# Kernel tuning notes

Hardware: AMD Instinct MI355X
Metric: run time of the kernel (lower is better)

The kernel has to match this reference:

```python
import jax, jax.numpy as jnp
import numpy as np

EMB_LEN = 16384
EMB_DIM = 128
BETA = 0.25
WEIGHT_DECAY = 0.01


def resize_linear(x, axis, out_size):
    # PyTorch (tri)linear interpolation, align_corners=False, separable per axis.
    in_size = x.shape[axis]
    if in_size == out_size:
        return x
    src = (jnp.arange(out_size, dtype=jnp.float32) + 0.5) * (in_size / out_size) - 0.5
    src = jnp.clip(src, 0.0, in_size - 1.0)
    i0 = jnp.floor(src).astype(jnp.int32)
    i1 = jnp.minimum(i0 + 1, in_size - 1)
    w1 = src - i0.astype(jnp.float32)
    x0 = jnp.take(x, i0, axis=axis)
    x1 = jnp.take(x, i1, axis=axis)
    bshape = [1] * x.ndim
    bshape[axis] = out_size
    w1 = w1.reshape(bshape)
    return x0 * (1.0 - w1) + x1 * w1


def setup_inputs() -> dict:
    key = jax.random.key(0)
    k1, k2 = jax.random.split(key)
    b, c, h, w = 16384, 16, 2, 4  # h*w must equal 8 (see shape analysis)
    z = jax.random.normal(k1, (b, c, h, w), dtype=jnp.float32)
    emb_weight = jax.random.uniform(
        k2, (EMB_LEN, EMB_DIM), dtype=jnp.float32,
        minval=-1.0 / EMB_LEN, maxval=1.0 / EMB_LEN)
    return {"z": z, "emb_weight": emb_weight}


def reference(z, emb_weight):
    b, c, h, w = z.shape
    # feature_unfolding: F.interpolate(x, 2, mode='trilinear') -> size=(2,2,2)
    x = z[:, :, None, :, :]                       # [b,c,1,h,w]
    x = resize_linear(x, 2, 2)                    # depth 1 -> 2 (duplicate)
    x = resize_linear(x, 3, 2)                    # h -> 2
    x = resize_linear(x, 4, 2)                    # w -> 2
    # pixelshuffle3D_downscale(scale=2) on [b,c,2,2,2] -> [b,8c,1,1,1];
    # flatten order matches contiguous reshape.
    zf = x.reshape(b, c * 8)                      # [b, emb_dim]
    # squared L2 distance via expansion
    d = (jnp.sum(zf ** 2, axis=1, keepdims=True)
         + jnp.sum(emb_weight ** 2, axis=1)
         - 2.0 * zf @ emb_weight.T)               # [b, emb_len]
    idx = jnp.argmin(d, axis=1)                   # [b]
    z_q = emb_weight[idx].reshape(b, c, h, w)
    sg = jax.lax.stop_gradient
    commit = BETA * jnp.mean((sg(z_q) - z) ** 2) + jnp.mean((z_q - sg(z)) ** 2)
    zd = sg(z)
    vx = z_q - jnp.mean(z_q)
    vy = zd - jnp.mean(zd)
    pearson = 0.5 + 0.5 * jnp.sum(vx * vy) / (
        jnp.sqrt(jnp.sum(vx ** 2)) * jnp.sqrt(jnp.sum(vy ** 2)))
    # torch.linalg.norm(W, ord=1) on 2D matrix = max column abs-sum
    reg = WEIGHT_DECAY * jnp.max(jnp.sum(jnp.abs(emb_weight), axis=0))
    loss = commit + pearson + reg
    z_q_out = z + sg(z_q - z)                     # straight-through
    # rearrange 'b h w c -> b c h w' on a [b,c,h,w] tensor == permute(0,3,1,2)
    z_q_out = jnp.transpose(z_q_out, (0, 3, 1, 2))
    return z_q_out, loss, idx
```

## Files before the change

### kernel.cpp

```cpp
#include <hip/hip_runtime.h>
#include <cstdint>
#include <cstddef>

#define B_ROWS 16384
#define EMB_LEN 16384
#define K_DIM 128
#define JSPLIT 8
#define JLEN (EMB_LEN / JSPLIT)
#define RB 32
#define JT 256
#define KC 16

typedef const __attribute__((address_space(1))) void* gas_vp;
typedef __attribute__((address_space(3))) void* las_vp;

__device__ __forceinline__ void dma16(const float* g, float* l) {
    __builtin_amdgcn_global_load_lds((gas_vp)g, (las_vp)l, 16, 0, 0);
}

__global__ void zf_kernel(const float* __restrict__ z,
                          float* __restrict__ zf, float* __restrict__ Cb) {
    int b = blockIdx.x;
    int i = threadIdx.x;
    int c = i >> 3, h = (i >> 1) & 1, wp = i & 1;
    const float* zr = z + (size_t)b * 128 + c * 8 + h * 4 + wp * 2;
    float v = 0.5f * zr[0] + 0.5f * zr[1];
    zf[(size_t)b * 128 + i] = v;
    float s = v * v;
    for (int o = 32; o; o >>= 1) s += __shfl_down(s, o, 64);
    __shared__ float sm[2];
    if ((threadIdx.x & 63) == 0) sm[threadIdx.x >> 6] = s;
    __syncthreads();
    if (threadIdx.x == 0) Cb[b] = sm[0] + sm[1];
}

__global__ void transpose_kernel(const float* __restrict__ emb,
                                 float* __restrict__ embT) {
    __shared__ float t[128][65];
    int j0 = blockIdx.x * 64;
    int jl = threadIdx.x >> 2;
    int kq = threadIdx.x & 3;
    const float* er = emb + (size_t)(j0 + jl) * 128;
#pragma unroll
    for (int q = 0; q < 8; ++q) {
        int k4 = (kq * 8 + q) * 4;
        float4 v = *(const float4*)(er + k4);
        t[k4 + 0][jl] = v.x;
        t[k4 + 1][jl] = v.y;
        t[k4 + 2][jl] = v.z;
        t[k4 + 3][jl] = v.w;
    }
    __syncthreads();
    int kk = threadIdx.x >> 4;
    int jl4 = (threadIdx.x & 15) * 4;
#pragma unroll
    for (int q = 0; q < 8; ++q) {
        int k = kk + q * 16;
        float4 v = make_float4(t[k][jl4], t[k][jl4 + 1], t[k][jl4 + 2], t[k][jl4 + 3]);
        *(float4*)(embT + (size_t)k * EMB_LEN + j0 + jl4) = v;
    }
}

#define FMA_ROW(cr, av) \
    cr.x = fmaf(av, bv.x, cr.x); \
    cr.y = fmaf(av, bv.y, cr.y); \
    cr.z = fmaf(av, bv.z, cr.z); \
    cr.w = fmaf(av, bv.w, cr.w);

#define UPD(rr, cr) { \
    float dv0 = cb##rr - 2.0f * cr.x; \
    float dv1 = cb##rr - 2.0f * cr.y; \
    float dv2 = cb##rr - 2.0f * cr.z; \
    float dv3 = cb##rr - 2.0f * cr.w; \
    if (dv0 < bd##rr) { bd##rr = dv0; bj##rr = jb; } \
    if (dv1 < bd##rr) { bd##rr = dv1; bj##rr = jb + 1; } \
    if (dv2 < bd##rr) { bd##rr = dv2; bj##rr = jb + 2; } \
    if (dv3 < bd##rr) { bd##rr = dv3; bj##rr = jb + 3; } \
}

#define RED(rr) { \
    float bd = bd##rr; int bj = bj##rr; \
    for (int o = 32; o; o >>= 1) { \
        float d2 = __shfl_down(bd, o, 64); \
        int j2 = __shfl_down(bj, o, 64); \
        if (d2 < bd || (d2 == bd && j2 < bj)) { bd = d2; bj = j2; } \
    } \
    if (l == 0) { \
        cand_d[sp * B_ROWS + rbase + w8 + rr] = bd; \
        cand_j[sp * B_ROWS + rbase + w8 + rr] = bj; \
    } \
}

__global__ void argmin_kernel(const float* __restrict__ zf,
                              const float* __restrict__ Cb,
                              const float* __restrict__ embT,
                              float* __restrict__ cand_d,
                              int* __restrict__ cand_j) {
    __shared__ float zfs[K_DIM][RB + 4];
    __shared__ float es[2][KC][JT];

    int sp = blockIdx.x & 7;
    int rb = blockIdx.x >> 3;
    int rbase = rb * RB;
    int jbase = sp * JLEN;
    int tid = threadIdx.x;
    int w = tid >> 6;
    int l = tid & 63;
    int w8 = w << 3;
    int l4 = l << 2;

    {
        int r0 = tid >> 3;
        int kq0 = tid & 7;
        const float* zr = zf + (size_t)(rbase + r0) * K_DIM;
        for (int kq = kq0; kq < 32; kq += 8) {
            float4 v = *(const float4*)(zr + kq * 4);
            zfs[kq * 4 + 0][r0] = v.x;
            zfs[kq * 4 + 1][r0] = v.y;
            zfs[kq * 4 + 2][r0] = v.z;
            zfs[kq * 4 + 3][r0] = v.w;
        }
    }

    const float* cbp = Cb + rbase + w8;
    float cb0 = cbp[0], cb1 = cbp[1], cb2 = cbp[2], cb3 = cbp[3];
    float cb4 = cbp[4], cb5 = cbp[5], cb6 = cbp[6], cb7 = cbp[7];

    float bd0 = 3.4e38f, bd1 = 3.4e38f, bd2 = 3.4e38f, bd3 = 3.4e38f;
    float bd4 = 3.4e38f, bd5 = 3.4e38f, bd6 = 3.4e38f, bd7 = 3.4e38f;
    int bj0 = 0, bj1 = 0, bj2 = 0, bj3 = 0, bj4 = 0, bj5 = 0, bj6 = 0, bj7 = 0;

    {
        const float* gb = embT + jbase + l4;
        float* lb = &es[0][w][0];
        dma16(gb + (size_t)(0 + w) * EMB_LEN, lb + 0 * JT);
        dma16(gb + (size_t)(4 + w) * EMB_LEN, lb + 4 * JT);
        dma16(gb + (size_t)(8 + w) * EMB_LEN, lb + 8 * JT);
        dma16(gb + (size_t)(12 + w) * EMB_LEN, lb + 12 * JT);
    }

    int buf = 0;
    for (int jt = 0; jt < JLEN; jt += JT) {
        float4 c0 = make_float4(0.f, 0.f, 0.f, 0.f);
        float4 c1 = make_float4(0.f, 0.f, 0.f, 0.f);
        float4 c2 = make_float4(0.f, 0.f, 0.f, 0.f);
        float4 c3 = make_float4(0.f, 0.f, 0.f, 0.f);
        float4 c4 = make_float4(0.f, 0.f, 0.f, 0.f);
        float4 c5 = make_float4(0.f, 0.f, 0.f, 0.f);
        float4 c6 = make_float4(0.f, 0.f, 0.f, 0.f);
        float4 c7 = make_float4(0.f, 0.f, 0.f, 0.f);

        for (int kc = 0; kc < K_DIM; kc += KC) {
            __syncthreads();

            {
                int kc2 = kc + KC, jt2 = jt;
                if (kc2 == K_DIM) { kc2 = 0; jt2 += JT; }
                if (jt2 < JLEN) {
                    const float* gb = embT + (size_t)kc2 * EMB_LEN + jbase + jt2 + l4;
                    float* lb = &es[buf ^ 1][w][0];
                    dma16(gb + (size_t)(0 + w) * EMB_LEN, lb + 0 * JT);
                    dma16(gb + (size_t)(4 + w) * EMB_LEN, lb + 4 * JT);
                    dma16(gb + (size_t)(8 + w) * EMB_LEN, lb + 8 * JT);
                    dma16(gb + (size_t)(12 + w) * EMB_LEN, lb + 12 * JT);
                }
            }

            const float (*eb)[JT] = es[buf];
#pragma unroll
            for (int k = 0; k < KC; ++k) {
                const float4 bv = *(const float4*)(&eb[k][l4]);
                const float4 a0 = *(const float4*)(&zfs[kc + k][w8]);
                const float4 a1 = *(const float4*)(&zfs[kc + k][w8 + 4]);
                FMA_ROW(c0, a0.x)
                FMA_ROW(c1, a0.y)
                FMA_ROW(c2, a0.z)
                FMA_ROW(c3, a0.w)
                FMA_ROW(c4, a1.x)
                FMA_ROW(c5, a1.y)
                FMA_ROW(c6, a1.z)
                FMA_ROW(c7, a1.w)
            }
            buf ^= 1;
        }

        int jb = jbase + jt + l4;
        UPD(0, c0)
        UPD(1, c1)
        UPD(2, c2)
        UPD(3, c3)
        UPD(4, c4)
        UPD(5, c5)
        UPD(6, c6)
        UPD(7, c7)
    }

    RED(0)
    RED(1)
    RED(2)
    RED(3)
    RED(4)
    RED(5)
    RED(6)
    RED(7)
}

__global__ void merge_kernel(const float* __restrict__ cand_d,
                             const int* __restrict__ cand_j,
                             int* __restrict__ idxw,
                             float* __restrict__ out_idx) {
    int b = blockIdx.x * 256 + threadIdx.x;
    float bd = cand_d[b];
    int bj = cand_j[b];
#pragma unroll
    for (int s = 1; s < JSPLIT; ++s) {
        float d = cand_d[s * B_ROWS + b];
        int j = cand_j[s * B_ROWS + b];
        if (d < bd) { bd = d; bj = j; }
    }
    idxw[b] = bj;
    out_idx[b] = (float)bj;
}

__global__ void output_kernel(const float* __restrict__ z,
                              const float* __restrict__ emb,
                              const int* __restrict__ idxw,
                              float* __restrict__ out,
                              double* __restrict__ accs) {
    int stride = gridDim.x * blockDim.x;
    double s[6] = {0, 0, 0, 0, 0, 0};
    for (int n = blockIdx.x * blockDim.x + threadIdx.x; n < B_ROWS * 128; n += stride) {
        int b = n >> 7, i = n & 127;
        int c = i >> 3, h = (i >> 2) & 1, w = i & 3;
        float zv = z[n];
        float qv = emb[(size_t)idxw[b] * 128 + i];
        float diff = qv - zv;
        out[(size_t)((b * 4 + w) * 16 + c) * 2 + h] = zv + diff;
        s[0] += (double)qv;
        s[1] += (double)zv;
        s[2] += (double)qv * qv;
        s[3] += (double)zv * zv;
        s[4] += (double)qv * zv;
        s[5] += (double)diff * diff;
    }
    int lane = threadIdx.x & 63, wv = threadIdx.x >> 6;
#pragma unroll
    for (int q = 0; q < 6; ++q)
        for (int o = 32; o; o >>= 1) s[q] += __shfl_down(s[q], o, 64);
    __shared__ double sm[6][4];
    if (lane == 0)
#pragma unroll
        for (int q = 0; q < 6; ++q) sm[q][wv] = s[q];
    __syncthreads();
    if (threadIdx.x == 0) {
#pragma unroll
        for (int q = 0; q < 6; ++q)
            atomicAdd(&accs[q], sm[q][0] + sm[q][1] + sm[q][2] + sm[q][3]);
    }
}

__global__ void colsum_kernel(const float* __restrict__ emb, float* __restrict__ colsum) {
    int j = blockIdx.x;
    double s = 0;
    for (int i = threadIdx.x; i < EMB_LEN; i += blockDim.x)
        s += (double)fabsf(emb[(size_t)i * 128 + j]);
    int lane = threadIdx.x & 63, wv = threadIdx.x >> 6;
    for (int o = 32; o; o >>= 1) s += __shfl_down(s, o, 64);
    __shared__ double sm[4];
    if (lane == 0) sm[wv] = s;
    __syncthreads();
    if (threadIdx.x == 0) colsum[j] = (float)(sm[0] + sm[1] + sm[2] + sm[3]);
}

__global__ void loss_kernel(const double* __restrict__ accs,
                            const float* __restrict__ colsum,
                            float* __restrict__ out_loss) {
    __shared__ float sm[128];
    int tid = threadIdx.x;
    sm[tid] = colsum[tid];
    __syncthreads();
    for (int s = 64; s; s >>= 1) {
        if (tid < s) sm[tid] = fmaxf(sm[tid], sm[tid + s]);
        __syncthreads();
    }
    if (tid == 0) {
        double n = (double)B_ROWS * 128.0;
        double m = accs[5] / n;
        double commit = 0.25 * m + m;
        double Sx = accs[0], Sy = accs[1], Sxx = accs[2], Syy = accs[3], Sxy = accs[4];
        double cov = Sxy - Sx * Sy / n;
        double vx = Sxx - Sx * Sx / n;
        double vy = Syy - Sy * Sy / n;
        double pearson = 0.5 + 0.5 * cov / (sqrt(vx) * sqrt(vy));
        double reg = 0.01 * (double)sm[0];
        out_loss[0] = (float)(commit + pearson + reg);
    }
}

extern "C" void kernel_launch(void* const* d_in, const int* in_sizes, int n_in,
                              void* d_out, int out_size, void* d_ws, size_t ws_size,
                              hipStream_t stream) {
    const float* z = (const float*)d_in[0];
    const float* emb = (const float*)d_in[1];
    float* out = (float*)d_out;

    float* zf = (float*)d_ws;
    float* embT = zf + 2097152;
    float* Cb = embT + 2097152;
    float* cand_d = Cb + 16384;
    int* cand_j = (int*)(cand_d + JSPLIT * B_ROWS);
    int* idxw = cand_j + JSPLIT * B_ROWS;
    double* accs = (double*)(idxw + 16384);
    float* colsum = (float*)(accs + 8);

    hipMemsetAsync(accs, 0, 8 * sizeof(double), stream);

    zf_kernel<<<B_ROWS, 128, 0, stream>>>(z, zf, Cb);
    transpose_kernel<<<EMB_LEN / 64, 256, 0, stream>>>(emb, embT);
    argmin_kernel<<<512 * JSPLIT, 256, 0, stream>>>(zf, Cb, embT, cand_d, cand_j);
    merge_kernel<<<B_ROWS / 256, 256, 0, stream>>>(cand_d, cand_j, idxw, out + 2097153);
    output_kernel<<<1024, 256, 0, stream>>>(z, emb, idxw, out, accs);
    colsum_kernel<<<128, 256, 0, stream>>>(emb, colsum);
    loss_kernel<<<1, 128, 0, stream>>>(accs, colsum, out + 2097152);
}
```

Baseline: 990.7 us.

## Enlarge argmin register tile to 16 rows per wave with KC halved

Doubles the rows handled per block (RB 32→64), so each wave keeps a 16×4 accumulator tile instead of 8×4. Each loaded embedding value is reused across twice as many rows, halving global embedding traffic per row. KC drops to 8 to keep the LDS footprint in check, and the per-row norms move to shared memory to save registers. The cost is higher register pressure (64 accumulators plus 16 best-distance/index pairs), which lowers occupancy, and twice as many barriers per tile.

```diff
diff --git a/kernel.cpp b/kernel.cpp
--- a/kernel.cpp
+++ b/kernel.cpp
@@ -7,9 +7,9 @@
 #define K_DIM 128
 #define JSPLIT 8
 #define JLEN (EMB_LEN / JSPLIT)
-#define RB 32
+#define RB 64
 #define JT 256
-#define KC 16
+#define KC 8
 
 typedef const __attribute__((address_space(1))) void* gas_vp;
 typedef __attribute__((address_space(3))) void* las_vp;
@@ -68,10 +68,11 @@
     cr.w = fmaf(av, bv.w, cr.w);
 
 #define UPD(rr, cr) { \
-    float dv0 = cb##rr - 2.0f * cr.x; \
-    float dv1 = cb##rr - 2.0f * cr.y; \
-    float dv2 = cb##rr - 2.0f * cr.z; \
-    float dv3 = cb##rr - 2.0f * cr.w; \
+    float cbr = cbs[w16 + rr]; \
+    float dv0 = cbr - 2.0f * cr.x; \
+    float dv1 = cbr - 2.0f * cr.y; \
+    float dv2 = cbr - 2.0f * cr.z; \
+    float dv3 = cbr - 2.0f * cr.w; \
     if (dv0 < bd##rr) { bd##rr = dv0; bj##rr = jb; } \
     if (dv1 < bd##rr) { bd##rr = dv1; bj##rr = jb + 1; } \
     if (dv2 < bd##rr) { bd##rr = dv2; bj##rr = jb + 2; } \
@@ -86,8 +87,8 @@
         if (d2 < bd || (d2 == bd && j2 < bj)) { bd = d2; bj = j2; } \
     } \
     if (l == 0) { \
-        cand_d[sp * B_ROWS + rbase + w8 + rr] = bd; \
-        cand_j[sp * B_ROWS + rbase + w8 + rr] = bj; \
+        cand_d[sp * B_ROWS + rbase + w16 + rr] = bd; \
+        cand_j[sp * B_ROWS + rbase + w16 + rr] = bj; \
     } \
 }
 
@@ -98,6 +99,7 @@
                               int* __restrict__ cand_j) {
     __shared__ float zfs[K_DIM][RB + 4];
     __shared__ float es[2][KC][JT];
+    __shared__ float cbs[RB];
 
     int sp = blockIdx.x & 7;
     int rb = blockIdx.x >> 3;
@@ -106,37 +108,34 @@
     int tid = threadIdx.x;
     int w = tid >> 6;
     int l = tid & 63;
-    int w8 = w << 3;
+    int w16 = w << 4;
     int l4 = l << 2;
 
     {
-        int r0 = tid >> 3;
-        int kq0 = tid & 7;
+        int r0 = tid >> 2;
+        int kq0 = tid & 3;
         const float* zr = zf + (size_t)(rbase + r0) * K_DIM;
-        for (int kq = kq0; kq < 32; kq += 8) {
+        for (int kq = kq0; kq < 32; kq += 4) {
             float4 v = *(const float4*)(zr + kq * 4);
             zfs[kq * 4 + 0][r0] = v.x;
             zfs[kq * 4 + 1][r0] = v.y;
             zfs[kq * 4 + 2][r0] = v.z;
             zfs[kq * 4 + 3][r0] = v.w;
         }
-    }
-
-    const float* cbp = Cb + rbase + w8;
-    float cb0 = cbp[0], cb1 = cbp[1], cb2 = cbp[2], cb3 = cbp[3];
-    float cb4 = cbp[4], cb5 = cbp[5], cb6 = cbp[6], cb7 = cbp[7];
+        if (tid < RB) cbs[tid] = Cb[rbase + tid];
+    }
 
     float bd0 = 3.4e38f, bd1 = 3.4e38f, bd2 = 3.4e38f, bd3 = 3.4e38f;
     float bd4 = 3.4e38f, bd5 = 3.4e38f, bd6 = 3.4e38f, bd7 = 3.4e38f;
+    float bd8 = 3.4e38f, bd9 = 3.4e38f, bd10 = 3.4e38f, bd11 = 3.4e38f;
+    float bd12 = 3.4e38f, bd13 = 3.4e38f, bd14 = 3.4e38f, bd15 = 3.4e38f;
     int bj0 = 0, bj1 = 0, bj2 = 0, bj3 = 0, bj4 = 0, bj5 = 0, bj6 = 0, bj7 = 0;
+    int bj8 = 0, bj9 = 0, bj10 = 0, bj11 = 0, bj12 = 0, bj13 = 0, bj14 = 0, bj15 = 0;
 
     {
         const float* gb = embT + jbase + l4;
-        float* lb = &es[0][w][0];
-        dma16(gb + (size_t)(0 + w) * EMB_LEN, lb + 0 * JT);
-        dma16(gb + (size_t)(4 + w) * EMB_LEN, lb + 4 * JT);
-        dma16(gb + (size_t)(8 + w) * EMB_LEN, lb + 8 * JT);
-        dma16(gb + (size_t)(12 + w) * EMB_LEN, lb + 12 * JT);
+        dma16(gb + (size_t)(2 * w) * EMB_LEN, &es[0][2 * w][0]);
+        dma16(gb + (size_t)(2 * w + 1) * EMB_LEN, &es[0][2 * w + 1][0]);
     }
 
     int buf = 0;
@@ -149,6 +148,14 @@
         float4 c5 = make_float4(0.f, 0.f, 0.f, 0.f);
         float4 c6 = make_float4(0.f, 0.f, 0.f, 0.f);
         float4 c7 = make_float4(0.f, 0.f, 0.f, 0.f);
+        float4 c8 = make_float4(0.f, 0.f, 0.f, 0.f);
+        float4 c9 = make_float4(0.f, 0.f, 0.f, 0.f);
+        float4 c10 = make_float4(0.f, 0.f, 0.f, 0.f);
+        float4 c11 = make_float4(0.f, 0.f, 0.f, 0.f);
+        float4 c12 = make_float4(0.f, 0.f, 0.f, 0.f);
+        float4 c13 = make_float4(0.f, 0.f, 0.f, 0.f);
+        float4 c14 = make_float4(0.f, 0.f, 0.f, 0.f);
+        float4 c15 = make_float4(0.f, 0.f, 0.f, 0.f);
 
         for (int kc = 0; kc < K_DIM; kc += KC) {
             __syncthreads();
@@ -158,11 +165,8 @@
                 if (kc2 == K_DIM) { kc2 = 0; jt2 += JT; }
                 if (jt2 < JLEN) {
                     const float* gb = embT + (size_t)kc2 * EMB_LEN + jbase + jt2 + l4;
-                    float* lb = &es[buf ^ 1][w][0];
-                    dma16(gb + (size_t)(0 + w) * EMB_LEN, lb + 0 * JT);
-                    dma16(gb + (size_t)(4 + w) * EMB_LEN, lb + 4 * JT);
-                    dma16(gb + (size_t)(8 + w) * EMB_LEN, lb + 8 * JT);
-                    dma16(gb + (size_t)(12 + w) * EMB_LEN, lb + 12 * JT);
+                    dma16(gb + (size_t)(2 * w) * EMB_LEN, &es[buf ^ 1][2 * w][0]);
+                    dma16(gb + (size_t)(2 * w + 1) * EMB_LEN, &es[buf ^ 1][2 * w + 1][0]);
                 }
             }
 
@@ -170,8 +174,10 @@
 #pragma unroll
             for (int k = 0; k < KC; ++k) {
                 const float4 bv = *(const float4*)(&eb[k][l4]);
-                const float4 a0 = *(const float4*)(&zfs[kc + k][w8]);
-                const float4 a1 = *(const float4*)(&zfs[kc + k][w8 + 4]);
+                const float4 a0 = *(const float4*)(&zfs[kc + k][w16]);
+                const float4 a1 = *(const float4*)(&zfs[kc + k][w16 + 4]);
+                const float4 a2 = *(const float4*)(&zfs[kc + k][w16 + 8]);
+                const float4 a3 = *(const float4*)(&zfs[kc + k][w16 + 12]);
                 FMA_ROW(c0, a0.x)
                 FMA_ROW(c1, a0.y)
                 FMA_ROW(c2, a0.z)
@@ -180,6 +186,14 @@
                 FMA_ROW(c5, a1.y)
                 FMA_ROW(c6, a1.z)
                 FMA_ROW(c7, a1.w)
+                FMA_ROW(c8, a2.x)
+                FMA_ROW(c9, a2.y)
+                FMA_ROW(c10, a2.z)
+                FMA_ROW(c11, a2.w)
+                FMA_ROW(c12, a3.x)
+                FMA_ROW(c13, a3.y)
+                FMA_ROW(c14, a3.z)
+                FMA_ROW(c15, a3.w)
             }
             buf ^= 1;
         }
@@ -193,6 +207,14 @@
         UPD(5, c5)
         UPD(6, c6)
         UPD(7, c7)
+        UPD(8, c8)
+        UPD(9, c9)
+        UPD(10, c10)
+        UPD(11, c11)
+        UPD(12, c12)
+        UPD(13, c13)
+        UPD(14, c14)
+        UPD(15, c15)
     }
 
     RED(0)
@@ -203,6 +225,14 @@
     RED(5)
     RED(6)
     RED(7)
+    RED(8)
+    RED(9)
+    RED(10)
+    RED(11)
+    RED(12)
+    RED(13)
+    RED(14)
+    RED(15)
 }
 
 __global__ void merge_kernel(const float* __restrict__ cand_d,
@@ -317,7 +347,7 @@
 
     zf_kernel<<<B_ROWS, 128, 0, stream>>>(z, zf, Cb);
     transpose_kernel<<<EMB_LEN / 64, 256, 0, stream>>>(emb, embT);
-    argmin_kernel<<<512 * JSPLIT, 256, 0, stream>>>(zf, Cb, embT, cand_d, cand_j);
+    argmin_kernel<<<(B_ROWS / RB) * JSPLIT, 256, 0, stream>>>(zf, Cb, embT, cand_d, cand_j);
     merge_kernel<<<B_ROWS / 256, 256, 0, stream>>>(cand_d, cand_j, idxw, out + 2097153);
     output_kernel<<<1024, 256, 0, stream>>>(z, emb, idxw, out, accs);
     colsum_kernel<<<128, 256, 0, stream>>>(emb, colsum);
```

New measurement: 1.076 ms. +8.6%, slower.
